# Kernel tuning notes

Hardware: AMD Instinct MI355X
Metric: run time of the kernel (lower is better)

Reference implementation:

```python
import jax, jax.numpy as jnp
import numpy as np

B, F, N, NO = 1, 512, 8192, 21
L1, L2, L3 = 640, 256, 128


def setup_inputs() -> dict:
    key = jax.random.key(0)
    ks = jax.random.split(key, 32)
    rn = lambda k, s: jax.random.normal(k, s, dtype=jnp.float32)
    inp = {
        "emb1": rn(ks[0], (B, F, N)),
        "emb2": rn(ks[1], (B, F, N)),
        "t1": rn(ks[2], (B, 3, N)),
        "t2": rn(ks[3], (B, 3, N)),
        "obj": jax.random.randint(ks[4], (B, 1), 0, NO, dtype=jnp.int32),
    }
    # 1x1 Conv1d weights == dense (out,in) matrices + bias
    dims_r = [(L1, 2 * F), (L2, L1), (L3, L2), (NO * 4, L3)]
    dims_t = [(L1, 2 * F), (L2, L1), (L3, L2), (NO * 3, L3)]
    ki = 5
    for br, dims in (("r", dims_r), ("t", dims_t)):
        for i, (o, c) in enumerate(dims, start=1):
            inp[f"w{i}{br}"] = rn(ks[ki], (o, c)) * (1.0 / np.sqrt(c)); ki += 1
            inp[f"b{i}{br}"] = rn(ks[ki], (o,)) * 0.01; ki += 1
    return inp


def _knn1(ref, qry):
    # ref, qry: (3, N). For each query point j, index of nearest ref point.
    g = ref.T @ qry  # (N_ref, N_qry)
    d2 = jnp.sum(ref * ref, axis=0)[:, None] + jnp.sum(qry * qry, axis=0)[None, :] - 2.0 * g
    return jnp.argmin(d2, axis=0)  # (N_qry,)


def _branch(x, w1, b1, w2, b2, w3, b3, w4, b4):
    h = jax.nn.relu(w1 @ x + b1[:, None])
    h = jax.nn.relu(w2 @ h + b2[:, None])
    h = jax.nn.relu(w3 @ h + b3[:, None])
    return w4 @ h + b4[:, None]


def reference(emb1, emb2, t1, t2, obj,
              w1r, b1r, w2r, b2r, w3r, b3r, w4r, b4r,
              w1t, b1t, w2t, b2t, w3t, b3t, w4t, b4t):
    bs, num_feat, num_points = emb1.shape
    t1 = t1.reshape(bs, 3, -1)
    t2 = t2.reshape(bs, 3, -1)
    # brute-force 1-NN of each t2 point among t1 points (bs == 1)
    idx = _knn1(t1[0], t2[0])  # (N,) zero-based (torch code subtracts 1 from 1-based inds)
    emb1g = emb1[0][:, idx]  # gather matched features, (F, N)
    # torch.stack([emb1,emb2],dim=1).view(bs, 2F, N) == channel concat [emb1g; emb2]
    emb = jnp.concatenate([emb1g, emb2[0]], axis=0)  # (2F, N)
    rx = _branch(emb, w1r, b1r, w2r, b2r, w3r, b3r, w4r, b4r).reshape(NO, 4, num_points)
    tx = _branch(emb, w1t, b1t, w2t, b2t, w3t, b3t, w4t, b4t).reshape(NO, 3, num_points)
    obj0 = obj[0]  # (1,)
    out_rx = jnp.transpose(rx[obj0], (0, 2, 1))  # (1, N, 4)
    out_tx = jnp.transpose(tx[obj0], (0, 2, 1))  # (1, N, 3)
    return out_rx, out_tx
```

## Files before the change

kernel.cpp:

```cpp
#include <hip/hip_runtime.h>

typedef unsigned short u16;
typedef __bf16 bf16x8 __attribute__((ext_vector_type(8)));
typedef float f32x4 __attribute__((ext_vector_type(4)));

__device__ __forceinline__ float b2f(u16 v) {
    return __uint_as_float(((unsigned int)v) << 16);
}
__device__ __forceinline__ u16 f2b(float f) {
    unsigned int u = __float_as_uint(f);
    u += 0x7fffu + ((u >> 16) & 1u);
    return (u16)(u >> 16);
}

__device__ __forceinline__ void ld_lds16(const u16* g, u16* l) {
    __builtin_amdgcn_global_load_lds(
        (__attribute__((address_space(1))) void*)(uintptr_t)(const void*)g,
        (__attribute__((address_space(3))) void*)l, 16, 0, 0);
}

__global__ void pack_w_k(const float* __restrict__ w1r, const float* __restrict__ w1t,
                         const float* __restrict__ w2r, const float* __restrict__ w2t,
                         const float* __restrict__ w3r, const float* __restrict__ w3t,
                         u16* __restrict__ dst)
{
    size_t i = (size_t)blockIdx.x * 2048 + (size_t)threadIdx.x * 8;
    const float* src; size_t off;
    if (i < 655360)       { src = w1r; off = 0; }
    else if (i < 1310720) { src = w1t; off = 655360; }
    else if (i < 1474560) { src = w2r; off = 1310720; }
    else if (i < 1638400) { src = w2t; off = 1474560; }
    else if (i < 1671168) { src = w3r; off = 1638400; }
    else                  { src = w3t; off = 1671168; }
    const float4 lo = *(const float4*)(src + (i - off));
    const float4 hi = *(const float4*)(src + (i - off) + 4);
    ushort4 o0, o1;
    o0.x = f2b(lo.x); o0.y = f2b(lo.y); o0.z = f2b(lo.z); o0.w = f2b(lo.w);
    o1.x = f2b(hi.x); o1.y = f2b(hi.y); o1.z = f2b(hi.z); o1.w = f2b(hi.w);
    *(ushort4*)(dst + i) = o0;
    *(ushort4*)(dst + i + 4) = o1;
}

__global__ void knn_k(const float* __restrict__ t1, const float* __restrict__ t2,
                      unsigned long long* __restrict__ keys)
{
    __shared__ float4 ref[128];
    const int t = threadIdx.x;
    const int rs = blockIdx.x;
    const int qb = blockIdx.y;
    if (t < 128) {
        int i = rs * 128 + t;
        float x = t1[i], y = t1[8192 + i], z = t1[16384 + i];
        float rr = __fadd_rn(__fadd_rn(__fmul_rn(x, x), __fmul_rn(y, y)), __fmul_rn(z, z));
        ref[t] = make_float4(x, y, z, rr);
    }
    __syncthreads();

    float qx[8], qy[8], qz[8], qq[8], bestd[8];
    int besti[8];
    const int q0 = qb * 2048 + t;
#pragma unroll
    for (int j = 0; j < 8; ++j) {
        int q = q0 + j * 256;
        qx[j] = t2[q]; qy[j] = t2[8192 + q]; qz[j] = t2[16384 + q];
        qq[j] = __fadd_rn(__fadd_rn(__fmul_rn(qx[j], qx[j]), __fmul_rn(qy[j], qy[j])),
                          __fmul_rn(qz[j], qz[j]));
        bestd[j] = __uint_as_float(0x7f800000u);
        besti[j] = 0;
    }
    for (int i = 0; i < 128; ++i) {
        float4 r = ref[i];
        int ridx = rs * 128 + i;
#pragma unroll
        for (int j = 0; j < 8; ++j) {
            float g = __fmaf_rn(qz[j], r.z, __fmaf_rn(qy[j], r.y, __fmul_rn(qx[j], r.x)));
            float d2 = __fsub_rn(__fadd_rn(r.w, qq[j]), __fmul_rn(2.0f, g));
            if (d2 < bestd[j]) { bestd[j] = d2; besti[j] = ridx; }
        }
    }
#pragma unroll
    for (int j = 0; j < 8; ++j) {
        unsigned long long key =
            ((unsigned long long)__float_as_uint(bestd[j]) << 32) | (unsigned int)besti[j];
        atomicMin(&keys[q0 + j * 256], key);
    }
}

__global__ void transpose_k(const float* __restrict__ e1, const float* __restrict__ e2,
                            u16* __restrict__ o1, u16* __restrict__ o2)
{
    __shared__ float tile[64][66];
    const float* in = blockIdx.z ? e2 : e1;
    u16* out = blockIdx.z ? o2 : o1;
    const int ostride = blockIdx.z ? 1024 : 512;
    const int coff = blockIdx.z ? 512 : 0;
    const int t = threadIdx.x;
    const int n0 = blockIdx.x * 64, f0 = blockIdx.y * 64;
    const int c = t & 63, r4 = t >> 6;
#pragma unroll
    for (int p = 0; p < 16; ++p) {
        int fr = p * 4 + r4;
        tile[fr][c] = in[(size_t)(f0 + fr) * 8192 + n0 + c];
    }
    __syncthreads();
#pragma unroll
    for (int p = 0; p < 16; ++p) {
        int nr = p * 4 + r4;
        out[(size_t)(n0 + nr) * ostride + coff + f0 + c] = f2b(tile[c][nr]);
    }
}

__global__ void gather_k(const unsigned long long* __restrict__ keys,
                         const u16* __restrict__ emb1t, u16* __restrict__ Xt)
{
    const int t = threadIdx.x, w = t >> 6, l = t & 63;
    const int nbase = blockIdx.x * 32;
#pragma unroll
    for (int it = 0; it < 8; ++it) {
        int n = nbase + it * 4 + w;
        int i = (int)(keys[n] & 0xffffffffu);
        const uint4* src = (const uint4*)(emb1t + (size_t)i * 512);
        uint4* dst = (uint4*)(Xt + (size_t)n * 1024);
        dst[l] = src[l];
    }
}

template <int TN>
__global__ __launch_bounds__(256) void gemm_bt(
    const u16* __restrict__ Ar, const u16* __restrict__ At,
    const float* __restrict__ biasr, const float* __restrict__ biast,
    const u16* __restrict__ Bt, u16* __restrict__ Ct,
    int Mh, int K, int bstride, int b_step, int ostride, int relu)
{
    constexpr int NJ = TN / 32;
    __shared__ __align__(16) u16 lds_a[128 * 32];
    __shared__ __align__(16) u16 lds_b[TN * 32];

    const int t = threadIdx.x;
    const int n0 = blockIdx.x * TN;
    const int m0 = blockIdx.y * 128;
    const int branch = blockIdx.z;

    const u16* A = branch ? At : Ar;
    const float* bias = branch ? biast : biasr;
    const int b_off = branch * b_step;
    const int out_off = branch * Mh;

    const int w = t >> 6, l = t & 63;
    const int sr = l >> 2, sc = (l & 3) * 8;

    const u16* gA0 = A + (size_t)(m0 + w * 32 + sr) * K + sc;
    const u16* gA1 = gA0 + (size_t)16 * K;
    u16* lA0 = &lds_a[w * 1024];
    u16* lA1 = lA0 + 512;

    const u16* gB0;
    const u16* gB1 = nullptr;
    u16 *lB0, *lB1 = nullptr;
    if (TN == 128) {
        gB0 = Bt + (size_t)(n0 + w * 32 + sr) * bstride + b_off + sc;
        gB1 = gB0 + (size_t)16 * bstride;
        lB0 = &lds_b[w * 1024];
        lB1 = lB0 + 512;
    } else {
        gB0 = Bt + (size_t)(n0 + w * 16 + sr) * bstride + b_off + sc;
        lB0 = &lds_b[w * 512];
    }

    const int wm = (w & 1) * 64;
    const int wn = (w >> 1) * (TN / 2);
    const int lrow = l & 15, quad = l >> 4;
    const u16* fa = &lds_a[(wm + lrow) * 32 + quad * 8];
    const u16* fb = &lds_b[(wn + lrow) * 32 + quad * 8];

    f32x4 acc[4][NJ];
#pragma unroll
    for (int i = 0; i < 4; ++i)
#pragma unroll
        for (int j = 0; j < NJ; ++j)
            acc[i][j] = (f32x4){0.f, 0.f, 0.f, 0.f};

    ld_lds16(gA0, lA0); ld_lds16(gA1, lA1);
    ld_lds16(gB0, lB0);
    if (TN == 128) ld_lds16(gB1, lB1);

    for (int kt = 0; kt < K; kt += 32) {
        __syncthreads();
        bf16x8 af[4], bfr[NJ];
#pragma unroll
        for (int i = 0; i < 4; ++i) af[i] = *(const bf16x8*)(fa + i * 16 * 32);
#pragma unroll
        for (int j = 0; j < NJ; ++j) bfr[j] = *(const bf16x8*)(fb + j * 16 * 32);
        __syncthreads();
        if (kt + 32 < K) {
            gA0 += 32; gA1 += 32; gB0 += 32;
            ld_lds16(gA0, lA0); ld_lds16(gA1, lA1);
            ld_lds16(gB0, lB0);
            if (TN == 128) { gB1 += 32; ld_lds16(gB1, lB1); }
        }
#pragma unroll
        for (int i = 0; i < 4; ++i)
#pragma unroll
            for (int j = 0; j < NJ; ++j)
                acc[i][j] = __builtin_amdgcn_mfma_f32_16x16x32_bf16(
                    af[i], bfr[j], acc[i][j], 0, 0, 0);
    }

#pragma unroll
    for (int i = 0; i < 4; ++i) {
        const int mbase = m0 + wm + i * 16 + quad * 4;
        const float4 bbv = *(const float4*)&bias[mbase];
#pragma unroll
        for (int j = 0; j < NJ; ++j) {
            const int n = n0 + wn + j * 16 + lrow;
            f32x4 v = acc[i][j];
            float x0 = v[0] + bbv.x, x1 = v[1] + bbv.y;
            float x2 = v[2] + bbv.z, x3 = v[3] + bbv.w;
            if (relu) {
                x0 = fmaxf(x0, 0.f); x1 = fmaxf(x1, 0.f);
                x2 = fmaxf(x2, 0.f); x3 = fmaxf(x3, 0.f);
            }
            ushort4 o;
            o.x = f2b(x0); o.y = f2b(x1); o.z = f2b(x2); o.w = f2b(x3);
            *(ushort4*)&Ct[(size_t)n * ostride + out_off + mbase] = o;
        }
    }
}

__global__ void final_k(const u16* __restrict__ h3t,
                        const float* __restrict__ w4r, const float* __restrict__ b4r,
                        const float* __restrict__ w4t, const float* __restrict__ b4t,
                        const int* __restrict__ objp, float* __restrict__ out)
{
    __shared__ float wr[4 * 128], wt[3 * 128], bb[7];
    const int t = threadIdx.x;
    const int o = objp[0];
    if (t < 128) {
#pragma unroll
        for (int r = 0; r < 4; ++r) wr[r * 128 + t] = w4r[(o * 4 + r) * 128 + t];
#pragma unroll
        for (int r = 0; r < 3; ++r) wt[r * 128 + t] = w4t[(o * 3 + r) * 128 + t];
    } else if (t < 135) {
        int r = t - 128;
        bb[r] = (r < 4) ? b4r[o * 4 + r] : b4t[o * 3 + (r - 4)];
    }
    __syncthreads();

    const int n = blockIdx.x * 256 + t;
    const u16* hp = h3t + (size_t)n * 256;
    float ar0 = 0, ar1 = 0, ar2 = 0, ar3 = 0, at0 = 0, at1 = 0, at2 = 0;
#pragma unroll
    for (int k = 0; k < 128; k += 8) {
        uint4 hv = *(const uint4*)(hp + k);
        const u16* hs = (const u16*)&hv;
        uint4 gv = *(const uint4*)(hp + 128 + k);
        const u16* gs = (const u16*)&gv;
#pragma unroll
        for (int j = 0; j < 8; ++j) {
            float h = b2f(hs[j]);
            ar0 = fmaf(h, wr[k + j], ar0);
            ar1 = fmaf(h, wr[128 + k + j], ar1);
            ar2 = fmaf(h, wr[256 + k + j], ar2);
            ar3 = fmaf(h, wr[384 + k + j], ar3);
            float g = b2f(gs[j]);
            at0 = fmaf(g, wt[k + j], at0);
            at1 = fmaf(g, wt[128 + k + j], at1);
            at2 = fmaf(g, wt[256 + k + j], at2);
        }
    }
    float4 ro = make_float4(ar0 + bb[0], ar1 + bb[1], ar2 + bb[2], ar3 + bb[3]);
    *(float4*)&out[n * 4] = ro;
    float* tp = out + 32768 + n * 3;
    tp[0] = at0 + bb[4]; tp[1] = at1 + bb[5]; tp[2] = at2 + bb[6];
}

extern "C" void kernel_launch(void* const* d_in, const int* in_sizes, int n_in,
                              void* d_out, int out_size, void* d_ws, size_t ws_size,
                              hipStream_t stream)
{
    const float* emb1 = (const float*)d_in[0];
    const float* emb2 = (const float*)d_in[1];
    const float* t1   = (const float*)d_in[2];
    const float* t2   = (const float*)d_in[3];
    const int*   obj  = (const int*)d_in[4];
    const float* w1r = (const float*)d_in[5];  const float* b1r = (const float*)d_in[6];
    const float* w2r = (const float*)d_in[7];  const float* b2r = (const float*)d_in[8];
    const float* w3r = (const float*)d_in[9];  const float* b3r = (const float*)d_in[10];
    const float* w4r = (const float*)d_in[11]; const float* b4r = (const float*)d_in[12];
    const float* w1t = (const float*)d_in[13]; const float* b1t = (const float*)d_in[14];
    const float* w2t = (const float*)d_in[15]; const float* b2t = (const float*)d_in[16];
    const float* w3t = (const float*)d_in[17]; const float* b3t = (const float*)d_in[18];
    const float* w4t = (const float*)d_in[19]; const float* b4t = (const float*)d_in[20];

    char* ws = (char*)d_ws;
    unsigned long long* keys = (unsigned long long*)ws;
    u16* emb1t = (u16*)(ws + (1u << 16));
    u16* Xt    = (u16*)(ws + (1u << 16) + (8u << 20));
    u16* h1t   = (u16*)(ws + (1u << 16) + (24u << 20));
    u16* wp    = (u16*)(ws + (1u << 16) + (44u << 20));
    u16* h2t   = emb1t;
    u16* h3t   = Xt;

    u16* w1rp = wp;            u16* w1tp = wp + 655360;
    u16* w2rp = wp + 1310720;  u16* w2tp = wp + 1474560;
    u16* w3rp = wp + 1638400;  u16* w3tp = wp + 1671168;

    hipMemsetAsync(keys, 0xFF, 8192 * sizeof(unsigned long long), stream);
    pack_w_k<<<832, 256, 0, stream>>>(w1r, w1t, w2r, w2t, w3r, w3t, wp);
    knn_k<<<dim3(64, 4), 256, 0, stream>>>(t1, t2, keys);
    transpose_k<<<dim3(128, 8, 2), 256, 0, stream>>>(emb1, emb2, emb1t, Xt);
    gather_k<<<256, 256, 0, stream>>>(keys, emb1t, Xt);
    gemm_bt<128><<<dim3(64, 5, 2), 256, 0, stream>>>(w1rp, w1tp, b1r, b1t, Xt,  h1t, 640, 1024, 1024,   0, 1280, 1);
    gemm_bt<64><<<dim3(128, 2, 2), 256, 0, stream>>>(w2rp, w2tp, b2r, b2t, h1t, h2t, 256,  640, 1280, 640,  512, 1);
    gemm_bt<64><<<dim3(128, 1, 2), 256, 0, stream>>>(w3rp, w3tp, b3r, b3t, h2t, h3t, 128,  256,  512, 256,  256, 1);
    final_k<<<32, 256, 0, stream>>>(h3t, w4r, b4r, w4t, b4t, obj, (float*)d_out);
}
```

Before: 210.5 us.

## Merge prep kernels and fuse kNN gather into first GEMM B-tile loads

Combines transpose, weight packing and kNN into one launch partitioned by block index. The separate gather kernel and the Xt buffer are removed: the first GEMM loads B tiles directly from the transposed emb1 rows selected by the kNN keys, or from emb2. Branch dispatch moves from blockIdx.z into the M dimension of the grid. This saves launches and the round-trip through the concatenated buffer, at the cost of scattered row reads inside the GEMM.

```diff
diff --git a/kernel.cpp b/kernel.cpp
--- a/kernel.cpp
+++ b/kernel.cpp
@@ -19,132 +19,202 @@
         (__attribute__((address_space(3))) void*)l, 16, 0, 0);
 }
 
-__global__ void pack_w_k(const float* __restrict__ w1r, const float* __restrict__ w1t,
-                         const float* __restrict__ w2r, const float* __restrict__ w2t,
-                         const float* __restrict__ w3r, const float* __restrict__ w3t,
-                         u16* __restrict__ dst)
-{
-    size_t i = (size_t)blockIdx.x * 2048 + (size_t)threadIdx.x * 8;
-    const float* src; size_t off;
-    if (i < 655360)       { src = w1r; off = 0; }
-    else if (i < 1310720) { src = w1t; off = 655360; }
-    else if (i < 1474560) { src = w2r; off = 1310720; }
-    else if (i < 1638400) { src = w2t; off = 1474560; }
-    else if (i < 1671168) { src = w3r; off = 1638400; }
-    else                  { src = w3t; off = 1671168; }
-    const float4 lo = *(const float4*)(src + (i - off));
-    const float4 hi = *(const float4*)(src + (i - off) + 4);
-    ushort4 o0, o1;
-    o0.x = f2b(lo.x); o0.y = f2b(lo.y); o0.z = f2b(lo.z); o0.w = f2b(lo.w);
-    o1.x = f2b(hi.x); o1.y = f2b(hi.y); o1.z = f2b(hi.z); o1.w = f2b(hi.w);
-    *(ushort4*)(dst + i) = o0;
-    *(ushort4*)(dst + i + 4) = o1;
-}
-
-__global__ void knn_k(const float* __restrict__ t1, const float* __restrict__ t2,
-                      unsigned long long* __restrict__ keys)
-{
-    __shared__ float4 ref[128];
+__global__ __launch_bounds__(256) void prep_k(
+    const float* __restrict__ emb1, const float* __restrict__ emb2,
+    const float* __restrict__ t1,   const float* __restrict__ t2,
+    const float* __restrict__ w1r, const float* __restrict__ w1t,
+    const float* __restrict__ w2r, const float* __restrict__ w2t,
+    const float* __restrict__ w3r, const float* __restrict__ w3t,
+    u16* __restrict__ e1t, u16* __restrict__ e2t, u16* __restrict__ wp,
+    unsigned long long* __restrict__ keys)
+{
+    __shared__ __align__(16) char smem[64 * 66 * 4];
+    const int bid = blockIdx.x;
     const int t = threadIdx.x;
-    const int rs = blockIdx.x;
-    const int qb = blockIdx.y;
-    if (t < 128) {
-        int i = rs * 128 + t;
-        float x = t1[i], y = t1[8192 + i], z = t1[16384 + i];
-        float rr = __fadd_rn(__fadd_rn(__fmul_rn(x, x), __fmul_rn(y, y)), __fmul_rn(z, z));
-        ref[t] = make_float4(x, y, z, rr);
-    }
-    __syncthreads();
-
-    float qx[8], qy[8], qz[8], qq[8], bestd[8];
-    int besti[8];
-    const int q0 = qb * 2048 + t;
-#pragma unroll
-    for (int j = 0; j < 8; ++j) {
-        int q = q0 + j * 256;
-        qx[j] = t2[q]; qy[j] = t2[8192 + q]; qz[j] = t2[16384 + q];
-        qq[j] = __fadd_rn(__fadd_rn(__fmul_rn(qx[j], qx[j]), __fmul_rn(qy[j], qy[j])),
-                          __fmul_rn(qz[j], qz[j]));
-        bestd[j] = __uint_as_float(0x7f800000u);
-        besti[j] = 0;
-    }
-    for (int i = 0; i < 128; ++i) {
-        float4 r = ref[i];
-        int ridx = rs * 128 + i;
+
+    if (bid < 2048) {
+        float (*tile)[66] = (float(*)[66])smem;
+        const int z = bid >> 10, rem = bid & 1023;
+        const float* in = z ? emb2 : emb1;
+        u16* out = z ? e2t : e1t;
+        const int n0 = (rem & 127) * 64, f0 = (rem >> 7) * 64;
+        const int c = t & 63, r4 = t >> 6;
+#pragma unroll
+        for (int p = 0; p < 16; ++p) {
+            int fr = p * 4 + r4;
+            tile[fr][c] = in[(size_t)(f0 + fr) * 8192 + n0 + c];
+        }
+        __syncthreads();
+#pragma unroll
+        for (int p = 0; p < 16; ++p) {
+            int nr = p * 4 + r4;
+            out[(size_t)(n0 + nr) * 512 + f0 + c] = f2b(tile[c][nr]);
+        }
+    } else if (bid < 2880) {
+        size_t i = (size_t)(bid - 2048) * 2048 + (size_t)t * 8;
+        const float* src; size_t off;
+        if (i < 655360)       { src = w1r; off = 0; }
+        else if (i < 1310720) { src = w1t; off = 655360; }
+        else if (i < 1474560) { src = w2r; off = 1310720; }
+        else if (i < 1638400) { src = w2t; off = 1474560; }
+        else if (i < 1671168) { src = w3r; off = 1638400; }
+        else                  { src = w3t; off = 1671168; }
+        const float4 lo = *(const float4*)(src + (i - off));
+        const float4 hi = *(const float4*)(src + (i - off) + 4);
+        ushort4 o0, o1;
+        o0.x = f2b(lo.x); o0.y = f2b(lo.y); o0.z = f2b(lo.z); o0.w = f2b(lo.w);
+        o1.x = f2b(hi.x); o1.y = f2b(hi.y); o1.z = f2b(hi.z); o1.w = f2b(hi.w);
+        *(ushort4*)(wp + i) = o0;
+        *(ushort4*)(wp + i + 4) = o1;
+    } else {
+        float4* ref = (float4*)smem;
+        const int kid = bid - 2880;
+        const int rs = kid & 63, qb = kid >> 6;
+        if (t < 128) {
+            int i = rs * 128 + t;
+            float x = t1[i], y = t1[8192 + i], z = t1[16384 + i];
+            float rr = __fadd_rn(__fadd_rn(__fmul_rn(x, x), __fmul_rn(y, y)),
+                                 __fmul_rn(z, z));
+            ref[t] = make_float4(x, y, z, rr);
+        }
+        __syncthreads();
+        float qx[8], qy[8], qz[8], qq[8], bestd[8];
+        int besti[8];
+        const int q0 = qb * 2048 + t;
 #pragma unroll
         for (int j = 0; j < 8; ++j) {
-            float g = __fmaf_rn(qz[j], r.z, __fmaf_rn(qy[j], r.y, __fmul_rn(qx[j], r.x)));
-            float d2 = __fsub_rn(__fadd_rn(r.w, qq[j]), __fmul_rn(2.0f, g));
-            if (d2 < bestd[j]) { bestd[j] = d2; besti[j] = ridx; }
-        }
-    }
-#pragma unroll
-    for (int j = 0; j < 8; ++j) {
-        unsigned long long key =
-            ((unsigned long long)__float_as_uint(bestd[j]) << 32) | (unsigned int)besti[j];
-        atomicMin(&keys[q0 + j * 256], key);
-    }
-}
-
-__global__ void transpose_k(const float* __restrict__ e1, const float* __restrict__ e2,
-                            u16* __restrict__ o1, u16* __restrict__ o2)
-{
-    __shared__ float tile[64][66];
-    const float* in = blockIdx.z ? e2 : e1;
-    u16* out = blockIdx.z ? o2 : o1;
-    const int ostride = blockIdx.z ? 1024 : 512;
-    const int coff = blockIdx.z ? 512 : 0;
+            int q = q0 + j * 256;
+            qx[j] = t2[q]; qy[j] = t2[8192 + q]; qz[j] = t2[16384 + q];
+            qq[j] = __fadd_rn(__fadd_rn(__fmul_rn(qx[j], qx[j]),
+                                        __fmul_rn(qy[j], qy[j])),
+                              __fmul_rn(qz[j], qz[j]));
+            bestd[j] = __uint_as_float(0x7f800000u);
+            besti[j] = 0;
+        }
+        for (int i = 0; i < 128; ++i) {
+            float4 r = ref[i];
+            int ridx = rs * 128 + i;
+#pragma unroll
+            for (int j = 0; j < 8; ++j) {
+                float g = __fmaf_rn(qz[j], r.z,
+                          __fmaf_rn(qy[j], r.y, __fmul_rn(qx[j], r.x)));
+                float d2 = __fsub_rn(__fadd_rn(r.w, qq[j]), __fmul_rn(2.0f, g));
+                if (d2 < bestd[j]) { bestd[j] = d2; besti[j] = ridx; }
+            }
+        }
+#pragma unroll
+        for (int j = 0; j < 8; ++j) {
+            unsigned long long key =
+                ((unsigned long long)__float_as_uint(bestd[j]) << 32) |
+                (unsigned int)besti[j];
+            atomicMin(&keys[q0 + j * 256], key);
+        }
+    }
+}
+
+__global__ __launch_bounds__(256) void gemm1_k(
+    const u16* __restrict__ A,
+    const float* __restrict__ b1r, const float* __restrict__ b1t,
+    const unsigned long long* __restrict__ keys,
+    const u16* __restrict__ e1t, const u16* __restrict__ e2t,
+    u16* __restrict__ Ct)
+{
+    __shared__ __align__(16) u16 lds_a[128 * 32];
+    __shared__ __align__(16) u16 lds_b[128 * 32];
+
     const int t = threadIdx.x;
-    const int n0 = blockIdx.x * 64, f0 = blockIdx.y * 64;
-    const int c = t & 63, r4 = t >> 6;
-#pragma unroll
-    for (int p = 0; p < 16; ++p) {
-        int fr = p * 4 + r4;
-        tile[fr][c] = in[(size_t)(f0 + fr) * 8192 + n0 + c];
-    }
-    __syncthreads();
-#pragma unroll
-    for (int p = 0; p < 16; ++p) {
-        int nr = p * 4 + r4;
-        out[(size_t)(n0 + nr) * ostride + coff + f0 + c] = f2b(tile[c][nr]);
-    }
-}
-
-__global__ void gather_k(const unsigned long long* __restrict__ keys,
-                         const u16* __restrict__ emb1t, u16* __restrict__ Xt)
-{
-    const int t = threadIdx.x, w = t >> 6, l = t & 63;
-    const int nbase = blockIdx.x * 32;
-#pragma unroll
-    for (int it = 0; it < 8; ++it) {
-        int n = nbase + it * 4 + w;
-        int i = (int)(keys[n] & 0xffffffffu);
-        const uint4* src = (const uint4*)(emb1t + (size_t)i * 512);
-        uint4* dst = (uint4*)(Xt + (size_t)n * 1024);
-        dst[l] = src[l];
-    }
-}
-
-template <int TN>
+    const int n0 = blockIdx.x * 128;
+    const int m0 = blockIdx.y * 128;
+    const int w = t >> 6, l = t & 63;
+    const int sr = l >> 2, sc = (l & 3) * 8;
+
+    const u16* gA0 = A + (size_t)(m0 + w * 32 + sr) * 1024 + sc;
+    const u16* gA1 = gA0 + (size_t)16 * 1024;
+    u16* lA0 = &lds_a[w * 1024];
+    u16* lA1 = lA0 + 512;
+
+    const int r0 = n0 + w * 32 + sr, r1 = r0 + 16;
+    const int i0 = (int)(keys[r0] & 0xffffffffu);
+    const int i1 = (int)(keys[r1] & 0xffffffffu);
+    const u16* pI0 = e1t + (size_t)i0 * 512 + sc;
+    const u16* pI1 = e1t + (size_t)i1 * 512 + sc;
+    const u16* pD0 = e2t + (size_t)r0 * 512 + sc;
+    const u16* pD1 = e2t + (size_t)r1 * 512 + sc;
+    u16* lB0 = &lds_b[w * 1024];
+    u16* lB1 = lB0 + 512;
+
+    const int wm = (w & 1) * 64;
+    const int wn = (w >> 1) * 64;
+    const int lrow = l & 15, quad = l >> 4;
+    const u16* fa = &lds_a[(wm + lrow) * 32 + quad * 8];
+    const u16* fb = &lds_b[(wn + lrow) * 32 + quad * 8];
+
+    f32x4 acc[4][4];
+#pragma unroll
+    for (int i = 0; i < 4; ++i)
+#pragma unroll
+        for (int j = 0; j < 4; ++j)
+            acc[i][j] = (f32x4){0.f, 0.f, 0.f, 0.f};
+
+    ld_lds16(gA0, lA0); ld_lds16(gA1, lA1);
+    ld_lds16(pI0, lB0); ld_lds16(pI1, lB1);
+
+    for (int kt = 0; kt < 1024; kt += 32) {
+        __syncthreads();
+        bf16x8 af[4], bfr[4];
+#pragma unroll
+        for (int i = 0; i < 4; ++i) af[i] = *(const bf16x8*)(fa + i * 16 * 32);
+#pragma unroll
+        for (int j = 0; j < 4; ++j) bfr[j] = *(const bf16x8*)(fb + j * 16 * 32);
+        __syncthreads();
+        const int kn = kt + 32;
+        if (kn < 1024) {
+            gA0 += 32; gA1 += 32;
+            const u16* s0 = (kn < 512) ? pI0 + kn : pD0 + (kn - 512);
+            const u16* s1 = (kn < 512) ? pI1 + kn : pD1 + (kn - 512);
+            ld_lds16(gA0, lA0); ld_lds16(gA1, lA1);
+            ld_lds16(s0, lB0); ld_lds16(s1, lB1);
+        }
+#pragma unroll
+        for (int i = 0; i < 4; ++i)
+#pragma unroll
+            for (int j = 0; j < 4; ++j)
+                acc[i][j] = __builtin_amdgcn_mfma_f32_16x16x32_bf16(
+                    af[i], bfr[j], acc[i][j], 0, 0, 0);
+    }
+
+    const float* bias = (m0 < 640) ? b1r : b1t;
+    const int boff = (m0 < 640) ? 0 : 640;
+#pragma unroll
+    for (int i = 0; i < 4; ++i) {
+        const int mbase = m0 + wm + i * 16 + quad * 4;
+        const float4 bbv = *(const float4*)&bias[mbase - boff];
+#pragma unroll
+        for (int j = 0; j < 4; ++j) {
+            const int n = n0 + wn + j * 16 + lrow;
+            f32x4 v = acc[i][j];
+            float x0 = fmaxf(v[0] + bbv.x, 0.f), x1 = fmaxf(v[1] + bbv.y, 0.f);
+            float x2 = fmaxf(v[2] + bbv.z, 0.f), x3 = fmaxf(v[3] + bbv.w, 0.f);
+            ushort4 o;
+            o.x = f2b(x0); o.y = f2b(x1); o.z = f2b(x2); o.w = f2b(x3);
+            *(ushort4*)&Ct[(size_t)n * 1280 + mbase] = o;
+        }
+    }
+}
+
 __global__ __launch_bounds__(256) void gemm_bt(
-    const u16* __restrict__ Ar, const u16* __restrict__ At,
+    const u16* __restrict__ A,
     const float* __restrict__ biasr, const float* __restrict__ biast,
     const u16* __restrict__ Bt, u16* __restrict__ Ct,
-    int Mh, int K, int bstride, int b_step, int ostride, int relu)
-{
-    constexpr int NJ = TN / 32;
+    int Mb, int K, int bstride, int b_step, int ostride)
+{
     __shared__ __align__(16) u16 lds_a[128 * 32];
-    __shared__ __align__(16) u16 lds_b[TN * 32];
+    __shared__ __align__(16) u16 lds_b[64 * 32];
 
     const int t = threadIdx.x;
-    const int n0 = blockIdx.x * TN;
+    const int n0 = blockIdx.x * 64;
     const int m0 = blockIdx.y * 128;
-    const int branch = blockIdx.z;
-
-    const u16* A = branch ? At : Ar;
-    const float* bias = branch ? biast : biasr;
-    const int b_off = branch * b_step;
-    const int out_off = branch * Mh;
+    const int br = (m0 >= Mb);
 
     const int w = t >> 6, l = t & 63;
     const int sr = l >> 2, sc = (l & 3) * 8;
@@ -154,75 +224,61 @@
     u16* lA0 = &lds_a[w * 1024];
     u16* lA1 = lA0 + 512;
 
-    const u16* gB0;
-    const u16* gB1 = nullptr;
-    u16 *lB0, *lB1 = nullptr;
-    if (TN == 128) {
-        gB0 = Bt + (size_t)(n0 + w * 32 + sr) * bstride + b_off + sc;
-        gB1 = gB0 + (size_t)16 * bstride;
-        lB0 = &lds_b[w * 1024];
-        lB1 = lB0 + 512;
-    } else {
-        gB0 = Bt + (size_t)(n0 + w * 16 + sr) * bstride + b_off + sc;
-        lB0 = &lds_b[w * 512];
-    }
+    const u16* gB0 = Bt + (size_t)(n0 + w * 16 + sr) * bstride + br * b_step + sc;
+    u16* lB0 = &lds_b[w * 512];
 
     const int wm = (w & 1) * 64;
-    const int wn = (w >> 1) * (TN / 2);
+    const int wn = (w >> 1) * 32;
     const int lrow = l & 15, quad = l >> 4;
     const u16* fa = &lds_a[(wm + lrow) * 32 + quad * 8];
     const u16* fb = &lds_b[(wn + lrow) * 32 + quad * 8];
 
-    f32x4 acc[4][NJ];
+    f32x4 acc[4][2];
 #pragma unroll
     for (int i = 0; i < 4; ++i)
 #pragma unroll
-        for (int j = 0; j < NJ; ++j)
+        for (int j = 0; j < 2; ++j)
             acc[i][j] = (f32x4){0.f, 0.f, 0.f, 0.f};
 
     ld_lds16(gA0, lA0); ld_lds16(gA1, lA1);
     ld_lds16(gB0, lB0);
-    if (TN == 128) ld_lds16(gB1, lB1);
 
     for (int kt = 0; kt < K; kt += 32) {
         __syncthreads();
-        bf16x8 af[4], bfr[NJ];
+        bf16x8 af[4], bfr[2];
 #pragma unroll
         for (int i = 0; i < 4; ++i) af[i] = *(const bf16x8*)(fa + i * 16 * 32);
 #pragma unroll
-        for (int j = 0; j < NJ; ++j) bfr[j] = *(const bf16x8*)(fb + j * 16 * 32);
+        for (int j = 0; j < 2; ++j) bfr[j] = *(const bf16x8*)(fb + j * 16 * 32);
         __syncthreads();
         if (kt + 32 < K) {
             gA0 += 32; gA1 += 32; gB0 += 32;
             ld_lds16(gA0, lA0); ld_lds16(gA1, lA1);
             ld_lds16(gB0, lB0);
-            if (TN == 128) { gB1 += 32; ld_lds16(gB1, lB1); }
         }
 #pragma unroll
         for (int i = 0; i < 4; ++i)
 #pragma unroll
-            for (int j = 0; j < NJ; ++j)
+            for (int j = 0; j < 2; ++j)
                 acc[i][j] = __builtin_amdgcn_mfma_f32_16x16x32_bf16(
                     af[i], bfr[j], acc[i][j], 0, 0, 0);
     }
 
+    const float* bias = br ? biast : biasr;
+    const int boff = br * Mb;
 #pragma unroll
     for (int i = 0; i < 4; ++i) {
         const int mbase = m0 + wm + i * 16 + quad * 4;
-        const float4 bbv = *(const float4*)&bias[mbase];
-#pragma unroll
-        for (int j = 0; j < NJ; ++j) {
+        const float4 bbv = *(const float4*)&bias[mbase - boff];
+#pragma unroll
+        for (int j = 0; j < 2; ++j) {
             const int n = n0 + wn + j * 16 + lrow;
             f32x4 v = acc[i][j];
-            float x0 = v[0] + bbv.x, x1 = v[1] + bbv.y;
-            float x2 = v[2] + bbv.z, x3 = v[3] + bbv.w;
-            if (relu) {
-                x0 = fmaxf(x0, 0.f); x1 = fmaxf(x1, 0.f);
-                x2 = fmaxf(x2, 0.f); x3 = fmaxf(x3, 0.f);
-            }
+            float x0 = fmaxf(v[0] + bbv.x, 0.f), x1 = fmaxf(v[1] + bbv.y, 0.f);
+            float x2 = fmaxf(v[2] + bbv.z, 0.f), x3 = fmaxf(v[3] + bbv.w, 0.f);
             ushort4 o;
             o.x = f2b(x0); o.y = f2b(x1); o.z = f2b(x2); o.w = f2b(x3);
-            *(ushort4*)&Ct[(size_t)n * ostride + out_off + mbase] = o;
+            *(ushort4*)&Ct[(size_t)n * ostride + mbase] = o;
         }
     }
 }
@@ -294,24 +350,23 @@
 
     char* ws = (char*)d_ws;
     unsigned long long* keys = (unsigned long long*)ws;
-    u16* emb1t = (u16*)(ws + (1u << 16));
-    u16* Xt    = (u16*)(ws + (1u << 16) + (8u << 20));
-    u16* h1t   = (u16*)(ws + (1u << 16) + (24u << 20));
-    u16* wp    = (u16*)(ws + (1u << 16) + (44u << 20));
-    u16* h2t   = emb1t;
-    u16* h3t   = Xt;
-
-    u16* w1rp = wp;            u16* w1tp = wp + 655360;
-    u16* w2rp = wp + 1310720;  u16* w2tp = wp + 1474560;
-    u16* w3rp = wp + 1638400;  u16* w3tp = wp + 1671168;
+    u16* e1t = (u16*)(ws + (1u << 16));
+    u16* e2t = (u16*)(ws + (1u << 16) + (8u << 20));
+    u16* h1t = (u16*)(ws + (1u << 16) + (16u << 20));
+    u16* h2t = (u16*)(ws + (1u << 16) + (36u << 20));
+    u16* h3t = (u16*)(ws + (1u << 16) + (44u << 20));
+    u16* wp  = (u16*)(ws + (1u << 16) + (48u << 20));
+
+    u16* w1p = wp;
+    u16* w2p = wp + 1310720;
+    u16* w3p = wp + 1638400;
 
     hipMemsetAsync(keys, 0xFF, 8192 * sizeof(unsigned long long), stream);
-    pack_w_k<<<832, 256, 0, stream>>>(w1r, w1t, w2r, w2t, w3r, w3t, wp);
-    knn_k<<<dim3(64, 4), 256, 0, stream>>>(t1, t2, keys);
-    transpose_k<<<dim3(128, 8, 2), 256, 0, stream>>>(emb1, emb2, emb1t, Xt);
-    gather_k<<<256, 256, 0, stream>>>(keys, emb1t, Xt);
-    gemm_bt<128><<<dim3(64, 5, 2), 256, 0, stream>>>(w1rp, w1tp, b1r, b1t, Xt,  h1t, 640, 1024, 1024,   0, 1280, 1);
-    gemm_bt<64><<<dim3(128, 2, 2), 256, 0, stream>>>(w2rp, w2tp, b2r, b2t, h1t, h2t, 256,  640, 1280, 640,  512, 1);
-    gemm_bt<64><<<dim3(128, 1, 2), 256, 0, stream>>>(w3rp, w3tp, b3r, b3t, h2t, h3t, 128,  256,  512, 256,  256, 1);
+    prep_k<<<3136, 256, 0, stream>>>(emb1, emb2, t1, t2,
+                                     w1r, w1t, w2r, w2t, w3r, w3t,
+                                     e1t, e2t, wp, keys);
+    gemm1_k<<<dim3(64, 10), 256, 0, stream>>>(w1p, b1r, b1t, keys, e1t, e2t, h1t);
+    gemm_bt<<<dim3(128, 4), 256, 0, stream>>>(w2p, b2r, b2t, h1t, h2t, 256, 640, 1280, 640, 512);
+    gemm_bt<<<dim3(128, 2), 256, 0, stream>>>(w3p, b3r, b3t, h2t, h3t, 128, 256, 512, 256, 256);
     final_k<<<32, 256, 0, stream>>>(h3t, w4r, b4r, w4t, b4t, obj, (float*)d_out);
 }
```

Measured after the change: 223.9 us. +6.4%, slower.
